# Kernel optimization log

Hardware: AMD Instinct MI355X
Metric: run time of the kernel (lower is better)

## Reference

```python
import jax, jax.numpy as jnp
import numpy as np


def setup_inputs() -> dict:
    key = jax.random.key(0)
    ks = jax.random.split(key, 5)
    B, H, W, dim = 2, 56, 56, 256
    heads, k = 8, 7
    s = 0.02
    return {
        "hidden_states": jax.random.normal(ks[0], (B, H, W, dim), jnp.float32),
        "wq": jax.random.normal(ks[1], (dim, dim), jnp.float32) * s,
        "bq": jnp.zeros((dim,), jnp.float32),
        "wk": jax.random.normal(ks[2], (dim, dim), jnp.float32) * s,
        "bk": jnp.zeros((dim,), jnp.float32),
        "wv": jax.random.normal(ks[3], (dim, dim), jnp.float32) * s,
        "bv": jnp.zeros((dim,), jnp.float32),
        "rpb": jax.random.normal(ks[4], (heads, 2 * k - 1, 2 * k - 1), jnp.float32) * s,
    }


def _window_start(L, k):
    # NATTEN window start for dilation=1: centered window, clamped to stay inside [0, L)
    ns = k // 2
    i = jnp.arange(L)
    return jnp.maximum(i - ns, 0) + jnp.where(i + ns >= L, L - i - ns - 1, 0)


def _neighborhood_attention(hidden_states, wq, bq, wk, bk, wv, bv, rpb):
    B, H, W, dim = hidden_states.shape
    heads = rpb.shape[0]
    k = (rpb.shape[1] + 1) // 2  # rpb is (heads, 2k-1, 2k-1)
    hd = dim // heads

    def proj(w, b):
        y = hidden_states @ w.T + b  # nn.Linear convention: x @ W^T + b
        return y.reshape(B, H, W, heads, hd).transpose(0, 3, 1, 2, 4)  # [B,h,H,W,d]

    q = proj(wq, bq) / jnp.sqrt(jnp.float32(hd))
    kl = proj(wk, bk)
    vl = proj(wv, bv)

    off = jnp.arange(k)
    ki = _window_start(H, k)[:, None] + off[None, :]  # [H,k] key row indices per query row
    kj = _window_start(W, k)[:, None] + off[None, :]  # [W,k] key col indices per query col

    def gather_nbhd(x):
        # x: [B,h,H,W,d] -> [B,h,H,W,k*k,d]
        g = x[:, :, ki[:, :, None, None], kj[None, None, :, :], :]  # [B,h,H,k,W,k,d]
        return g.transpose(0, 1, 2, 4, 3, 5, 6).reshape(B, heads, H, W, k * k, hd)

    kn = gather_nbhd(kl)
    vn = gather_nbhd(vl)

    # relative position bias index = (key_pos - query_pos) + (k - 1)
    pbi = ki - jnp.arange(H)[:, None] + (k - 1)  # [H,k]
    pbj = kj - jnp.arange(W)[:, None] + (k - 1)  # [W,k]
    bias = rpb[:, pbi[:, :, None, None], pbj[None, None, :, :]]  # [h,H,k,W,k]
    bias = bias.transpose(0, 1, 3, 2, 4).reshape(heads, H, W, k * k)

    scores = jnp.einsum('bnijd,bnijkd->bnijk', q, kn) + bias[None]
    probs = jax.nn.softmax(scores, axis=-1)  # dropout prob = 0.0 (eval)
    ctx = jnp.einsum('bnijk,bnijkd->bnijd', probs, vn)
    return ctx.transpose(0, 2, 3, 1, 4).reshape(B, H, W, dim)


def reference(hidden_states, wq, bq, wk, bk, wv, bv, rpb):
    return _neighborhood_attention(hidden_states, wq, bq, wk, bk, wv, bv, rpb)
```

## Files before the change

### kernel.cpp

```cpp
#include <hip/hip_runtime.h>
#include <hip/hip_bf16.h>

typedef __attribute__((ext_vector_type(8))) short bf16x8;
typedef __attribute__((ext_vector_type(4))) float f32x4;

#define NPIX 6272
#define HW 56
#define HEADS 8
#define HD 32
#define KW 7
#define DIM 256
#define GDIM 768
#define UK 112
#define UKP 128
#define NX (NPIX * DIM)
#define NW (DIM * DIM)

__device__ inline short f2bf(float f) {
    __hip_bfloat16 h = __float2bfloat16(f);
    return *(short*)&h;
}
__device__ inline float bf2f(short u) {
    union { unsigned int i; float f; } x;
    x.i = ((unsigned int)(unsigned short)u) << 16;
    return x.f;
}

__device__ __forceinline__ void gl_lds16(const short* g, short* l) {
    __builtin_amdgcn_global_load_lds(
        (const __attribute__((address_space(1))) unsigned int*)g,
        (__attribute__((address_space(3))) unsigned int*)l,
        16, 0, 0);
}

__global__ __launch_bounds__(256) void cvt_kernel(
    const float* __restrict__ X,
    const float* __restrict__ Wq, const float* __restrict__ Wk, const float* __restrict__ Wv,
    short* __restrict__ Xb, short* __restrict__ Wcb)
{
    const size_t e0 = ((size_t)blockIdx.x * 256 + threadIdx.x) * 8;
    const float* src; short* dst; size_t off;
    if (e0 < NX)                { src = X;  dst = Xb;        off = e0; }
    else if (e0 < NX + NW)      { src = Wq; dst = Wcb;       off = e0 - NX; }
    else if (e0 < NX + 2 * NW)  { src = Wk; dst = Wcb + NW;  off = e0 - NX - NW; }
    else                        { src = Wv; dst = Wcb + 2*NW; off = e0 - NX - 2 * NW; }
    float4 f0 = *(const float4*)(src + off);
    float4 f1 = *(const float4*)(src + off + 4);
    bf16x8 v;
    v[0]=f2bf(f0.x); v[1]=f2bf(f0.y); v[2]=f2bf(f0.z); v[3]=f2bf(f0.w);
    v[4]=f2bf(f1.x); v[5]=f2bf(f1.y); v[6]=f2bf(f1.z); v[7]=f2bf(f1.w);
    *(bf16x8*)(dst + off) = v;
}

__global__ __launch_bounds__(256, 2) void proj_kernel(
    const short* __restrict__ Xb,
    const short* __restrict__ Wcb,
    const float* __restrict__ Bq, const float* __restrict__ Bk, const float* __restrict__ Bv,
    short* __restrict__ Y)
{
    __shared__ short Ash[64 * 256];
    __shared__ short Bsh[64 * 256];

    const int id   = blockIdx.x;
    const int flat = (id & 7) * 147 + (id >> 3);
    const int bx   = flat / 12;
    const int by   = flat - bx * 12;

    const int tid  = threadIdx.x;
    const int wave = tid >> 6;
    const int lane = tid & 63;
    const int l15  = lane & 15;
    const int hi   = lane >> 4;

    const int brow = bx * 64;
    const int bcol = by * 64;

    #pragma unroll
    for (int i = 0; i < 8; ++i) {
        const int slot = tid + i * 256;
        const int row  = slot >> 5;
        const int p    = slot & 31;
        const int goff = ((p ^ (row & 7)) << 3);
        gl_lds16(Xb  + (size_t)(brow + row) * DIM + goff, Ash + slot * 8);
        gl_lds16(Wcb + (size_t)(bcol + row) * DIM + goff, Bsh + slot * 8);
    }
    __syncthreads();

    f32x4 acc[4];
    #pragma unroll
    for (int c = 0; c < 4; ++c) acc[c] = (f32x4){0.f, 0.f, 0.f, 0.f};

    const int arow = wave * 16 + l15;
    #pragma unroll
    for (int kk = 0; kk < 8; ++kk) {
        const int ch = kk * 4 + hi;
        bf16x8 a = *(const bf16x8*)((char*)Ash + arow * 512 + ((ch ^ (arow & 7)) << 4));
        #pragma unroll
        for (int c = 0; c < 4; ++c) {
            const int bro = c * 16 + l15;
            bf16x8 b = *(const bf16x8*)((char*)Bsh + bro * 512 + ((ch ^ (bro & 7)) << 4));
            acc[c] = __builtin_amdgcn_mfma_f32_16x16x32_bf16(a, b, acc[c], 0, 0, 0);
        }
    }

    const int z = by >> 2;
    const float* Bi = (z == 0) ? Bq : (z == 1) ? Bk : Bv;
    const float scale = (z == 0) ? 0.17677669529663687f : 1.0f;
    #pragma unroll
    for (int c = 0; c < 4; ++c) {
        const int ocol = bcol + c * 16 + l15;
        const float bvv = Bi[ocol & 255];
        #pragma unroll
        for (int r = 0; r < 4; ++r) {
            const int row = brow + wave * 16 + hi * 4 + r;
            Y[(size_t)row * GDIM + ocol] = f2bf((acc[c][r] + bvv) * scale);
        }
    }
}

__global__ __launch_bounds__(256, 3) void nattn_kernel(
    const short* __restrict__ Yg,
    const float* __restrict__ rpb,
    float* __restrict__ out)
{
    __shared__ short VshT[128 * UKP];
    __shared__ short Psh[4 * 16 * UKP];
    __shared__ __align__(16) short rpbs[8 * 169];

    const int id   = blockIdx.x;
    const int flat = (id & 7) * 98 + (id >> 3);
    const int bz   = flat / 392;
    int rem        = flat - bz * 392;
    const int ip   = rem / 14;
    rem           -= ip * 14;
    const int hg   = rem / 7;
    const int jt   = rem - hg * 7;

    const int tid  = threadIdx.x;
    const int wv   = tid >> 6;
    const int lane = tid & 63;
    const int l15  = lane & 15;
    const int hi   = lane >> 4;

    const int i0 = 2 * ip;
    const int j0 = jt * 8;
    const int r0 = min(max(i0 - 3, 0), HW - KW);
    const int c0 = min(max(j0 - 3, 0), HW - KW);

    const int h = hg * 4 + wv;

    const int k2   = tid & 63;
    const int dblk = tid >> 6;
    const int keyL = 2 * k2, keyR = 2 * k2 + 1;
    const int aL = keyL / 14, cL = keyL - aL * 14;
    const int aR = keyR / 14, cR = keyR - aR * 14;
    const int giL = min(r0 + aL, HW - 1), gjL = min(c0 + cL, HW - 1);
    const int giR = min(r0 + aR, HW - 1), gjR = min(c0 + cR, HW - 1);
    const short* srcL = Yg + (size_t)((bz * HW + giL) * HW + gjL) * GDIM + 512 + hg * 128 + dblk * 32;
    const short* srcR = Yg + (size_t)((bz * HW + giR) * HW + gjR) * GDIM + 512 + hg * 128 + dblk * 32;
    bf16x8 vL[4], vR[4];
    #pragma unroll
    for (int m = 0; m < 4; ++m) {
        vL[m] = (keyL < UK) ? *(const bf16x8*)(srcL + m * 8) : (bf16x8){0,0,0,0,0,0,0,0};
        vR[m] = (keyR < UK) ? *(const bf16x8*)(srcR + m * 8) : (bf16x8){0,0,0,0,0,0,0,0};
    }

    const int qpix = (bz * HW + i0 + (l15 >> 3)) * HW + j0 + (l15 & 7);
    bf16x8 aq = *(const bf16x8*)(Yg + (size_t)qpix * GDIM + h * HD + hi * 8);

    const float4* rpb4 = (const float4*)rpb;
    float4 rv0 = rpb4[tid];
    float4 rv1 = (tid < 338 - 256) ? rpb4[tid + 256] : (float4){0.f,0.f,0.f,0.f};

    #pragma unroll
    for (int m = 0; m < 4; ++m) {
        #pragma unroll
        for (int e = 0; e < 8; ++e) {
            const int d = dblk * 32 + m * 8 + e;
            const int w = ((int)(unsigned short)vL[m][e]) | ((int)vR[m][e] << 16);
            *(int*)((char*)VshT + d * 256 + ((4 * k2) ^ (e << 4))) = w;
        }
    }
    *(short4*)(&rpbs[tid * 4]) = make_short4(f2bf(rv0.x), f2bf(rv0.y), f2bf(rv0.z), f2bf(rv0.w));
    if (tid < 338 - 256)
        *(short4*)(&rpbs[(tid + 256) * 4]) = make_short4(f2bf(rv1.x), f2bf(rv1.y), f2bf(rv1.z), f2bf(rv1.w));
    {
        const int p = (lane >> 2) & 15, m4 = lane & 3;
        const int k = UK + m4 * 4;
        char* dst = (char*)Psh + (wv * 16 + p) * 256 + ((2 * k) ^ (p << 4));
        *(int2*)dst = make_int2(0, 0);
    }
    __syncthreads();

    int iv[4], jv[4], bb[4], uai[4], ucj[4];
    #pragma unroll
    for (int r = 0; r < 4; ++r) {
        const int p = hi * 4 + r;
        iv[r] = i0 + (p >> 3);
        jv[r] = j0 + (p & 7);
        const int siv = min(max(iv[r] - 3, 0), HW - KW);
        const int sjv = min(max(jv[r] - 3, 0), HW - KW);
        bb[r]  = (r0 - iv[r] + 6) * 13 + (c0 - jv[r] + 6);
        uai[r] = siv - r0;
        ucj[r] = sjv - c0;
    }
    const f32x4 zf = {0.f, 0.f, 0.f, 0.f};

    f32x4 sacc[7];
    {
        bf16x8 kb[7];
        #pragma unroll
        for (int t = 0; t < 7; ++t) {
            const int key = t * 16 + l15;
            const int a = key / 14, c = key - a * 14;
            const int gi = min(r0 + a, HW - 1), gj = min(c0 + c, HW - 1);
            kb[t] = *(const bf16x8*)(Yg + (size_t)((bz * HW + gi) * HW + gj) * GDIM +
                                     256 + h * HD + hi * 8);
        }
        #pragma unroll
        for (int t = 0; t < 7; ++t)
            sacc[t] = __builtin_amdgcn_mfma_f32_16x16x32_bf16(aq, kb[t], zf, 0, 0, 0);
    }

    const short* rbh = rpbs + h * 169;
    int aA[7], cA[7], a13[7];
    #pragma unroll
    for (int t = 0; t < 7; ++t) {
        const int key = t * 16 + l15;
        aA[t] = key / 14;
        cA[t] = key - aA[t] * 14;
        a13[t] = aA[t] * 13 + cA[t];
    }
    float sc[4][7];
    #pragma unroll
    for (int t = 0; t < 7; ++t) {
        #pragma unroll
        for (int r = 0; r < 4; ++r) {
            const bool ok = ((unsigned)(aA[t] - uai[r]) <= 6u) &
                            ((unsigned)(cA[t] - ucj[r]) <= 6u);
            const float s = sacc[t][r] + bf2f(rbh[bb[r] + a13[t]]);
            sc[r][t] = ok ? s : -1e30f;
        }
    }

    float sm[4];
    #pragma unroll
    for (int r = 0; r < 4; ++r) {
        float m = sc[r][0];
        #pragma unroll
        for (int t = 1; t < 7; ++t) m = fmaxf(m, sc[r][t]);
        m = fmaxf(m, __shfl_xor(m, 1));
        m = fmaxf(m, __shfl_xor(m, 2));
        m = fmaxf(m, __shfl_xor(m, 4));
        m = fmaxf(m, __shfl_xor(m, 8));
        const int pix = hi * 4 + r;
        char* prow = (char*)Psh + (wv * 16 + pix) * 256;
        const int pswz = pix << 4;
        float s = 0.f;
        #pragma unroll
        for (int t = 0; t < 7; ++t) {
            const float e = __expf(sc[r][t] - m);
            s += e;
            const int key = t * 16 + l15;
            *(short*)(prow + ((2 * key) ^ pswz)) = f2bf(e);
        }
        s += __shfl_xor(s, 1);
        s += __shfl_xor(s, 2);
        s += __shfl_xor(s, 4);
        s += __shfl_xor(s, 8);
        sm[r] = s;
    }

    const int d0 = wv * 32 + l15;
    f32x4 o0 = zf, o1 = zf;
    #pragma unroll
    for (int kk = 0; kk < 4; ++kk) {
        bf16x8 pa = *(const bf16x8*)((char*)Psh + (wv * 16 + l15) * 256 +
                                     ((kk * 64 + hi * 16) ^ (l15 << 4)));
        const int koff = (kk * 64 + hi * 16) ^ ((l15 & 7) << 4);
        bf16x8 vb0 = *(const bf16x8*)((char*)VshT + d0 * 256 + koff);
        bf16x8 vb1 = *(const bf16x8*)((char*)VshT + (d0 + 16) * 256 + koff);
        o0 = __builtin_amdgcn_mfma_f32_16x16x32_bf16(pa, vb0, o0, 0, 0, 0);
        o1 = __builtin_amdgcn_mfma_f32_16x16x32_bf16(pa, vb1, o1, 0, 0, 0);
    }

    #pragma unroll
    for (int r = 0; r < 4; ++r) {
        const float inv = 1.f / sm[r];
        const int pg = (bz * HW + iv[r]) * HW + jv[r];
        out[(size_t)pg * DIM + h * HD + l15]      = o0[r] * inv;
        out[(size_t)pg * DIM + h * HD + 16 + l15] = o1[r] * inv;
    }
}

extern "C" void kernel_launch(void* const* d_in, const int* in_sizes, int n_in,
                              void* d_out, int out_size, void* d_ws, size_t ws_size,
                              hipStream_t stream) {
    const float* hs = (const float*)d_in[0];
    const float* wq = (const float*)d_in[1];
    const float* bq = (const float*)d_in[2];
    const float* wk = (const float*)d_in[3];
    const float* bk = (const float*)d_in[4];
    const float* wv = (const float*)d_in[5];
    const float* bv = (const float*)d_in[6];
    const float* rpb = (const float*)d_in[7];

    short* Y   = (short*)d_ws;
    short* Xb  = Y + (size_t)NPIX * GDIM;
    short* Wcb = Xb + (size_t)NX;

    cvt_kernel<<<(NX + 3 * NW) / (256 * 8), 256, 0, stream>>>(hs, wq, wk, wv, Xb, Wcb);

    proj_kernel<<<1176, 256, 0, stream>>>(Xb, Wcb, bq, bk, bv, Y);

    nattn_kernel<<<784, 256, 0, stream>>>(Y, rpb, (float*)d_out);
}
```

Measured before the change: 32.80 us.

## Split projection K-loop into two staged halves and hoist K loads before barrier

The projection GEMM now loads the 256-wide K dimension as two 128-wide halves into separate LDS buffers. MFMA work on the first half can start while the second half's global-to-LDS copies are still in flight. In the attention kernel, the key-vector global loads are issued before the V-transpose/LDS staging and the barrier, so their latency overlaps with the shared-memory setup. This raises register pressure (kb held across the barrier) and adds an extra sync in the GEMM.

```diff
diff --git a/kernel.cpp b/kernel.cpp
--- a/kernel.cpp
+++ b/kernel.cpp
@@ -58,8 +58,8 @@
     const float* __restrict__ Bq, const float* __restrict__ Bk, const float* __restrict__ Bv,
     short* __restrict__ Y)
 {
-    __shared__ short Ash[64 * 256];
-    __shared__ short Bsh[64 * 256];
+    __shared__ short Ash[2][1024 * 8];
+    __shared__ short Bsh[2][1024 * 8];
 
     const int id   = blockIdx.x;
     const int flat = (id & 7) * 147 + (id >> 3);
@@ -75,30 +75,51 @@
     const int brow = bx * 64;
     const int bcol = by * 64;
 
-    #pragma unroll
-    for (int i = 0; i < 8; ++i) {
-        const int slot = tid + i * 256;
-        const int row  = slot >> 5;
-        const int p    = slot & 31;
+    f32x4 acc[4];
+    #pragma unroll
+    for (int c = 0; c < 4; ++c) acc[c] = (f32x4){0.f, 0.f, 0.f, 0.f};
+    const int arow = wave * 16 + l15;
+
+    #pragma unroll
+    for (int i = 0; i < 4; ++i) {
+        const int slot = i * 256 + tid;
+        const int row = slot >> 4, p = slot & 15;
         const int goff = ((p ^ (row & 7)) << 3);
-        gl_lds16(Xb  + (size_t)(brow + row) * DIM + goff, Ash + slot * 8);
-        gl_lds16(Wcb + (size_t)(bcol + row) * DIM + goff, Bsh + slot * 8);
+        gl_lds16(Xb  + (size_t)(brow + row) * DIM + goff, &Ash[0][slot * 8]);
+        gl_lds16(Wcb + (size_t)(bcol + row) * DIM + goff, &Bsh[0][slot * 8]);
     }
     __syncthreads();
 
-    f32x4 acc[4];
-    #pragma unroll
-    for (int c = 0; c < 4; ++c) acc[c] = (f32x4){0.f, 0.f, 0.f, 0.f};
-
-    const int arow = wave * 16 + l15;
-    #pragma unroll
-    for (int kk = 0; kk < 8; ++kk) {
+    #pragma unroll
+    for (int i = 0; i < 4; ++i) {
+        const int slot = i * 256 + tid;
+        const int row = slot >> 4, p = slot & 15;
+        const int goff = ((p ^ (row & 7)) << 3) + 128;
+        gl_lds16(Xb  + (size_t)(brow + row) * DIM + goff, &Ash[1][slot * 8]);
+        gl_lds16(Wcb + (size_t)(bcol + row) * DIM + goff, &Bsh[1][slot * 8]);
+    }
+
+    #pragma unroll
+    for (int kk = 0; kk < 4; ++kk) {
         const int ch = kk * 4 + hi;
-        bf16x8 a = *(const bf16x8*)((char*)Ash + arow * 512 + ((ch ^ (arow & 7)) << 4));
+        bf16x8 a = *(const bf16x8*)((char*)&Ash[0][0] + arow * 256 + ((ch ^ (arow & 7)) << 4));
         #pragma unroll
         for (int c = 0; c < 4; ++c) {
             const int bro = c * 16 + l15;
-            bf16x8 b = *(const bf16x8*)((char*)Bsh + bro * 512 + ((ch ^ (bro & 7)) << 4));
+            bf16x8 b = *(const bf16x8*)((char*)&Bsh[0][0] + bro * 256 + ((ch ^ (bro & 7)) << 4));
+            acc[c] = __builtin_amdgcn_mfma_f32_16x16x32_bf16(a, b, acc[c], 0, 0, 0);
+        }
+    }
+    __syncthreads();
+
+    #pragma unroll
+    for (int kk = 0; kk < 4; ++kk) {
+        const int ch = kk * 4 + hi;
+        bf16x8 a = *(const bf16x8*)((char*)&Ash[1][0] + arow * 256 + ((ch ^ (arow & 7)) << 4));
+        #pragma unroll
+        for (int c = 0; c < 4; ++c) {
+            const int bro = c * 16 + l15;
+            bf16x8 b = *(const bf16x8*)((char*)&Bsh[1][0] + bro * 256 + ((ch ^ (bro & 7)) << 4));
             acc[c] = __builtin_amdgcn_mfma_f32_16x16x32_bf16(a, b, acc[c], 0, 0, 0);
         }
     }
@@ -168,29 +189,19 @@
     const int qpix = (bz * HW + i0 + (l15 >> 3)) * HW + j0 + (l15 & 7);
     bf16x8 aq = *(const bf16x8*)(Yg + (size_t)qpix * GDIM + h * HD + hi * 8);
 
+    bf16x8 kb[7];
+    #pragma unroll
+    for (int t = 0; t < 7; ++t) {
+        const int key = t * 16 + l15;
+        const int a = key / 14, c = key - a * 14;
+        const int gi = min(r0 + a, HW - 1), gj = min(c0 + c, HW - 1);
+        kb[t] = *(const bf16x8*)(Yg + (size_t)((bz * HW + gi) * HW + gj) * GDIM +
+                                 256 + h * HD + hi * 8);
+    }
+
     const float4* rpb4 = (const float4*)rpb;
     float4 rv0 = rpb4[tid];
     float4 rv1 = (tid < 338 - 256) ? rpb4[tid + 256] : (float4){0.f,0.f,0.f,0.f};
-
-    #pragma unroll
-    for (int m = 0; m < 4; ++m) {
-        #pragma unroll
-        for (int e = 0; e < 8; ++e) {
-            const int d = dblk * 32 + m * 8 + e;
-            const int w = ((int)(unsigned short)vL[m][e]) | ((int)vR[m][e] << 16);
-            *(int*)((char*)VshT + d * 256 + ((4 * k2) ^ (e << 4))) = w;
-        }
-    }
-    *(short4*)(&rpbs[tid * 4]) = make_short4(f2bf(rv0.x), f2bf(rv0.y), f2bf(rv0.z), f2bf(rv0.w));
-    if (tid < 338 - 256)
-        *(short4*)(&rpbs[(tid + 256) * 4]) = make_short4(f2bf(rv1.x), f2bf(rv1.y), f2bf(rv1.z), f2bf(rv1.w));
-    {
-        const int p = (lane >> 2) & 15, m4 = lane & 3;
-        const int k = UK + m4 * 4;
-        char* dst = (char*)Psh + (wv * 16 + p) * 256 + ((2 * k) ^ (p << 4));
-        *(int2*)dst = make_int2(0, 0);
-    }
-    __syncthreads();
 
     int iv[4], jv[4], bb[4], uai[4], ucj[4];
     #pragma unroll
@@ -204,25 +215,6 @@
         uai[r] = siv - r0;
         ucj[r] = sjv - c0;
     }
-    const f32x4 zf = {0.f, 0.f, 0.f, 0.f};
-
-    f32x4 sacc[7];
-    {
-        bf16x8 kb[7];
-        #pragma unroll
-        for (int t = 0; t < 7; ++t) {
-            const int key = t * 16 + l15;
-            const int a = key / 14, c = key - a * 14;
-            const int gi = min(r0 + a, HW - 1), gj = min(c0 + c, HW - 1);
-            kb[t] = *(const bf16x8*)(Yg + (size_t)((bz * HW + gi) * HW + gj) * GDIM +
-                                     256 + h * HD + hi * 8);
-        }
-        #pragma unroll
-        for (int t = 0; t < 7; ++t)
-            sacc[t] = __builtin_amdgcn_mfma_f32_16x16x32_bf16(aq, kb[t], zf, 0, 0, 0);
-    }
-
-    const short* rbh = rpbs + h * 169;
     int aA[7], cA[7], a13[7];
     #pragma unroll
     for (int t = 0; t < 7; ++t) {
@@ -231,6 +223,35 @@
         cA[t] = key - aA[t] * 14;
         a13[t] = aA[t] * 13 + cA[t];
     }
+
+    #pragma unroll
+    for (int m = 0; m < 4; ++m) {
+        #pragma unroll
+        for (int e = 0; e < 8; ++e) {
+            const int d = dblk * 32 + m * 8 + e;
+            const int w = ((int)(unsigned short)vL[m][e]) | ((int)vR[m][e] << 16);
+            *(int*)((char*)VshT + d * 256 + ((4 * k2) ^ (e << 4))) = w;
+        }
+    }
+    *(short4*)(&rpbs[tid * 4]) = make_short4(f2bf(rv0.x), f2bf(rv0.y), f2bf(rv0.z), f2bf(rv0.w));
+    if (tid < 338 - 256)
+        *(short4*)(&rpbs[(tid + 256) * 4]) = make_short4(f2bf(rv1.x), f2bf(rv1.y), f2bf(rv1.z), f2bf(rv1.w));
+    {
+        const int p = (lane >> 2) & 15, m4 = lane & 3;
+        const int k = UK + m4 * 4;
+        char* dst = (char*)Psh + (wv * 16 + p) * 256 + ((2 * k) ^ (p << 4));
+        *(int2*)dst = make_int2(0, 0);
+    }
+    __syncthreads();
+
+    const f32x4 zf = {0.f, 0.f, 0.f, 0.f};
+
+    f32x4 sacc[7];
+    #pragma unroll
+    for (int t = 0; t < 7; ++t)
+        sacc[t] = __builtin_amdgcn_mfma_f32_16x16x32_bf16(aq, kb[t], zf, 0, 0, 0);
+
+    const short* rbh = rpbs + h * 169;
     float sc[4][7];
     #pragma unroll
     for (int t = 0; t < 7; ++t) {
```

After: 33.15 us. Within noise of the previous version (+1.1%).

## Store projected Q/K/V in head-planar layout for contiguous per-head reads

Applied to the files above, without the earlier changes.

The projection kernel now writes Q, K and V as separate per-head planes of 32-wide rows instead of one interleaved 768-wide row per pixel. The attention kernel's K, Q and V loads are rewritten against the new layout, and the V transpose into shared memory now writes individual shorts instead of packed pairs. The aim is to make neighbourhood gathers touch contiguous 64-byte rows per head for better cache-line use. In exchange, the projection epilogue writes are more scattered and the V staging issues more LDS stores.

```diff
diff --git a/kernel.cpp b/kernel.cpp
--- a/kernel.cpp
+++ b/kernel.cpp
@@ -10,7 +10,6 @@
 #define HD 32
 #define KW 7
 #define DIM 256
-#define GDIM 768
 #define UK 112
 #define UKP 128
 #define NX (NPIX * DIM)
@@ -108,12 +107,15 @@
     const float scale = (z == 0) ? 0.17677669529663687f : 1.0f;
     #pragma unroll
     for (int c = 0; c < 4; ++c) {
-        const int ocol = bcol + c * 16 + l15;
-        const float bvv = Bi[ocol & 255];
+        const int col256 = (by & 3) * 64 + c * 16 + l15;
+        const int h = col256 >> 5;
+        const int d = col256 & 31;
+        const float bvv = Bi[col256];
+        const size_t pbase = (size_t)(z * 8 + h) * NPIX;
         #pragma unroll
         for (int r = 0; r < 4; ++r) {
             const int row = brow + wave * 16 + hi * 4 + r;
-            Y[(size_t)row * GDIM + ocol] = f2bf((acc[c][r] + bvv) * scale);
+            Y[(pbase + row) * 32 + d] = f2bf((acc[c][r] + bvv) * scale);
         }
     }
 }
@@ -149,38 +151,34 @@
 
     const int h = hg * 4 + wv;
 
-    const int k2   = tid & 63;
-    const int dblk = tid >> 6;
-    const int keyL = 2 * k2, keyR = 2 * k2 + 1;
-    const int aL = keyL / 14, cL = keyL - aL * 14;
-    const int aR = keyR / 14, cR = keyR - aR * 14;
-    const int giL = min(r0 + aL, HW - 1), gjL = min(c0 + cL, HW - 1);
-    const int giR = min(r0 + aR, HW - 1), gjR = min(c0 + cR, HW - 1);
-    const short* srcL = Yg + (size_t)((bz * HW + giL) * HW + gjL) * GDIM + 512 + hg * 128 + dblk * 32;
-    const short* srcR = Yg + (size_t)((bz * HW + giR) * HW + gjR) * GDIM + 512 + hg * 128 + dblk * 32;
-    bf16x8 vL[4], vR[4];
-    #pragma unroll
-    for (int m = 0; m < 4; ++m) {
-        vL[m] = (keyL < UK) ? *(const bf16x8*)(srcL + m * 8) : (bf16x8){0,0,0,0,0,0,0,0};
-        vR[m] = (keyR < UK) ? *(const bf16x8*)(srcR + m * 8) : (bf16x8){0,0,0,0,0,0,0,0};
+    #pragma unroll
+    for (int hh = 0; hh < 4; ++hh) {
+        const size_t vpl = (size_t)(16 + hg * 4 + hh) * NPIX;
+        #pragma unroll
+        for (int i = 0; i < 2; ++i) {
+            const int slot  = i * 256 + tid;
+            const int key   = slot >> 2;
+            const int chunk = slot & 3;
+            const int a = key / 14, c = key - a * 14;
+            const int gi = min(r0 + a, HW - 1), gj = min(c0 + c, HW - 1);
+            bf16x8 vv = {0,0,0,0,0,0,0,0};
+            if (key < UK)
+                vv = *(const bf16x8*)(Yg + (vpl + (bz * HW + gi) * HW + gj) * 32 + chunk * 8);
+            #pragma unroll
+            for (int e = 0; e < 8; ++e) {
+                const int d = chunk * 8 + e;
+                *(short*)((char*)VshT + (hh * 32 + d) * 256 + ((2 * key) ^ (e << 4))) = vv[e];
+            }
+        }
     }
 
     const int qpix = (bz * HW + i0 + (l15 >> 3)) * HW + j0 + (l15 & 7);
-    bf16x8 aq = *(const bf16x8*)(Yg + (size_t)qpix * GDIM + h * HD + hi * 8);
+    bf16x8 aq = *(const bf16x8*)(Yg + ((size_t)h * NPIX + qpix) * 32 + hi * 8);
 
     const float4* rpb4 = (const float4*)rpb;
     float4 rv0 = rpb4[tid];
     float4 rv1 = (tid < 338 - 256) ? rpb4[tid + 256] : (float4){0.f,0.f,0.f,0.f};
 
-    #pragma unroll
-    for (int m = 0; m < 4; ++m) {
-        #pragma unroll
-        for (int e = 0; e < 8; ++e) {
-            const int d = dblk * 32 + m * 8 + e;
-            const int w = ((int)(unsigned short)vL[m][e]) | ((int)vR[m][e] << 16);
-            *(int*)((char*)VshT + d * 256 + ((4 * k2) ^ (e << 4))) = w;
-        }
-    }
     *(short4*)(&rpbs[tid * 4]) = make_short4(f2bf(rv0.x), f2bf(rv0.y), f2bf(rv0.z), f2bf(rv0.w));
     if (tid < 338 - 256)
         *(short4*)(&rpbs[(tid + 256) * 4]) = make_short4(f2bf(rv1.x), f2bf(rv1.y), f2bf(rv1.z), f2bf(rv1.w));
@@ -208,14 +206,14 @@
 
     f32x4 sacc[7];
     {
+        const size_t kpl = (size_t)(8 + h) * NPIX;
         bf16x8 kb[7];
         #pragma unroll
         for (int t = 0; t < 7; ++t) {
             const int key = t * 16 + l15;
             const int a = key / 14, c = key - a * 14;
             const int gi = min(r0 + a, HW - 1), gj = min(c0 + c, HW - 1);
-            kb[t] = *(const bf16x8*)(Yg + (size_t)((bz * HW + gi) * HW + gj) * GDIM +
-                                     256 + h * HD + hi * 8);
+            kb[t] = *(const bf16x8*)(Yg + (kpl + (bz * HW + gi) * HW + gj) * 32 + hi * 8);
         }
         #pragma unroll
         for (int t = 0; t < 7; ++t)
@@ -306,7 +304,7 @@
     const float* rpb = (const float*)d_in[7];
 
     short* Y   = (short*)d_ws;
-    short* Xb  = Y + (size_t)NPIX * GDIM;
+    short* Xb  = Y + (size_t)24 * NPIX * 32;
     short* Wcb = Xb + (size_t)NX;
 
     cvt_kernel<<<(NX + 3 * NW) / (256 * 8), 256, 0, stream>>>(hs, wq, wk, wv, Xb, Wcb);
```

Result: slower. 33.89 us (+3.3%).

## Transpose MFMA operands so softmax probabilities stay in registers, drop LDS staging

Applied to the files above, without the earlier changes.

The score and PV MFMAs now swap their operands, so each lane holds the scores for one query pixel across keys. The softmax reductions then need only two cross-lane shuffles, and the bf16 probabilities are packed and redistributed with __shfl instead of being written to and read back from a shared-memory P buffer. Removing that buffer cuts LDS use, which allows raising the launch-bounds occupancy hint from 3 to 4. Outputs are written as float4 vectors. The trade-off is extra shuffle and select instructions plus higher register pressure under the tighter occupancy bound.

```diff
diff --git a/kernel.cpp b/kernel.cpp
--- a/kernel.cpp
+++ b/kernel.cpp
@@ -118,13 +118,12 @@
     }
 }
 
-__global__ __launch_bounds__(256, 3) void nattn_kernel(
+__global__ __launch_bounds__(256, 4) void nattn_kernel(
     const short* __restrict__ Yg,
     const float* __restrict__ rpb,
     float* __restrict__ out)
 {
     __shared__ short VshT[128 * UKP];
-    __shared__ short Psh[4 * 16 * UKP];
     __shared__ __align__(16) short rpbs[8 * 169];
 
     const int id   = blockIdx.x;
@@ -184,26 +183,15 @@
     *(short4*)(&rpbs[tid * 4]) = make_short4(f2bf(rv0.x), f2bf(rv0.y), f2bf(rv0.z), f2bf(rv0.w));
     if (tid < 338 - 256)
         *(short4*)(&rpbs[(tid + 256) * 4]) = make_short4(f2bf(rv1.x), f2bf(rv1.y), f2bf(rv1.z), f2bf(rv1.w));
-    {
-        const int p = (lane >> 2) & 15, m4 = lane & 3;
-        const int k = UK + m4 * 4;
-        char* dst = (char*)Psh + (wv * 16 + p) * 256 + ((2 * k) ^ (p << 4));
-        *(int2*)dst = make_int2(0, 0);
-    }
     __syncthreads();
 
-    int iv[4], jv[4], bb[4], uai[4], ucj[4];
-    #pragma unroll
-    for (int r = 0; r < 4; ++r) {
-        const int p = hi * 4 + r;
-        iv[r] = i0 + (p >> 3);
-        jv[r] = j0 + (p & 7);
-        const int siv = min(max(iv[r] - 3, 0), HW - KW);
-        const int sjv = min(max(jv[r] - 3, 0), HW - KW);
-        bb[r]  = (r0 - iv[r] + 6) * 13 + (c0 - jv[r] + 6);
-        uai[r] = siv - r0;
-        ucj[r] = sjv - c0;
-    }
+    const int iv = i0 + (l15 >> 3);
+    const int jv = j0 + (l15 & 7);
+    const int siv = min(max(iv - 3, 0), HW - KW);
+    const int sjv = min(max(jv - 3, 0), HW - KW);
+    const int bb  = (r0 - iv + 6) * 13 + (c0 - jv + 6);
+    const int uai = siv - r0;
+    const int ucj = sjv - c0;
     const f32x4 zf = {0.f, 0.f, 0.f, 0.f};
 
     f32x4 sacc[7];
@@ -219,78 +207,78 @@
         }
         #pragma unroll
         for (int t = 0; t < 7; ++t)
-            sacc[t] = __builtin_amdgcn_mfma_f32_16x16x32_bf16(aq, kb[t], zf, 0, 0, 0);
+            sacc[t] = __builtin_amdgcn_mfma_f32_16x16x32_bf16(kb[t], aq, zf, 0, 0, 0);
     }
 
     const short* rbh = rpbs + h * 169;
-    int aA[7], cA[7], a13[7];
+    float sc[7][4];
     #pragma unroll
     for (int t = 0; t < 7; ++t) {
-        const int key = t * 16 + l15;
-        aA[t] = key / 14;
-        cA[t] = key - aA[t] * 14;
-        a13[t] = aA[t] * 13 + cA[t];
-    }
-    float sc[4][7];
+        #pragma unroll
+        for (int r = 0; r < 4; ++r) {
+            const int key = t * 16 + (hi << 2) + r;
+            const int a = key / 14, c = key - a * 14;
+            const bool ok = ((unsigned)(a - uai) <= 6u) & ((unsigned)(c - ucj) <= 6u);
+            const float s = sacc[t][r] + bf2f(rbh[bb + a * 13 + c]);
+            sc[t][r] = ok ? s : -1e30f;
+        }
+    }
+
+    float m = sc[0][0];
+    #pragma unroll
+    for (int t = 0; t < 7; ++t)
+        #pragma unroll
+        for (int r = 0; r < 4; ++r) m = fmaxf(m, sc[t][r]);
+    m = fmaxf(m, __shfl_xor(m, 16));
+    m = fmaxf(m, __shfl_xor(m, 32));
+
+    float sm = 0.f;
+    unsigned long long pk[7];
     #pragma unroll
     for (int t = 0; t < 7; ++t) {
-        #pragma unroll
-        for (int r = 0; r < 4; ++r) {
-            const bool ok = ((unsigned)(aA[t] - uai[r]) <= 6u) &
-                            ((unsigned)(cA[t] - ucj[r]) <= 6u);
-            const float s = sacc[t][r] + bf2f(rbh[bb[r] + a13[t]]);
-            sc[r][t] = ok ? s : -1e30f;
-        }
-    }
-
-    float sm[4];
-    #pragma unroll
-    for (int r = 0; r < 4; ++r) {
-        float m = sc[r][0];
-        #pragma unroll
-        for (int t = 1; t < 7; ++t) m = fmaxf(m, sc[r][t]);
-        m = fmaxf(m, __shfl_xor(m, 1));
-        m = fmaxf(m, __shfl_xor(m, 2));
-        m = fmaxf(m, __shfl_xor(m, 4));
-        m = fmaxf(m, __shfl_xor(m, 8));
-        const int pix = hi * 4 + r;
-        char* prow = (char*)Psh + (wv * 16 + pix) * 256;
-        const int pswz = pix << 4;
-        float s = 0.f;
-        #pragma unroll
-        for (int t = 0; t < 7; ++t) {
-            const float e = __expf(sc[r][t] - m);
-            s += e;
-            const int key = t * 16 + l15;
-            *(short*)(prow + ((2 * key) ^ pswz)) = f2bf(e);
-        }
-        s += __shfl_xor(s, 1);
-        s += __shfl_xor(s, 2);
-        s += __shfl_xor(s, 4);
-        s += __shfl_xor(s, 8);
-        sm[r] = s;
-    }
-
+        float e0 = __expf(sc[t][0] - m), e1 = __expf(sc[t][1] - m);
+        float e2 = __expf(sc[t][2] - m), e3 = __expf(sc[t][3] - m);
+        sm += (e0 + e1) + (e2 + e3);
+        const unsigned u0 = (unsigned)(unsigned short)f2bf(e0) |
+                            ((unsigned)(unsigned short)f2bf(e1) << 16);
+        const unsigned u1 = (unsigned)(unsigned short)f2bf(e2) |
+                            ((unsigned)(unsigned short)f2bf(e3) << 16);
+        pk[t] = (unsigned long long)u0 | ((unsigned long long)u1 << 32);
+    }
+    sm += __shfl_xor(sm, 16);
+    sm += __shfl_xor(sm, 32);
+
+    const int s0 = l15 + ((hi & 1) << 5);
+    const bool hiSel = (hi >> 1) & 1;
     const int d0 = wv * 32 + l15;
     f32x4 o0 = zf, o1 = zf;
     #pragma unroll
     for (int kk = 0; kk < 4; ++kk) {
-        bf16x8 pa = *(const bf16x8*)((char*)Psh + (wv * 16 + l15) * 256 +
-                                     ((kk * 64 + hi * 16) ^ (l15 << 4)));
+        unsigned long long a0 = __shfl(pk[2 * kk], s0, 64);
+        unsigned long long b0 = __shfl(pk[2 * kk], s0 + 16, 64);
+        unsigned long long a1 = 0ULL, b1 = 0ULL;
+        if (2 * kk + 1 < 7) {
+            a1 = __shfl(pk[2 * kk + 1], s0, 64);
+            b1 = __shfl(pk[2 * kk + 1], s0 + 16, 64);
+        }
+        bf16x8 pa;
+        ((unsigned long long*)&pa)[0] = hiSel ? a1 : a0;
+        ((unsigned long long*)&pa)[1] = hiSel ? b1 : b0;
+
         const int koff = (kk * 64 + hi * 16) ^ ((l15 & 7) << 4);
-        bf16x8 vb0 = *(const bf16x8*)((char*)VshT + d0 * 256 + koff);
-        bf16x8 vb1 = *(const bf16x8*)((char*)VshT + (d0 + 16) * 256 + koff);
-        o0 = __builtin_amdgcn_mfma_f32_16x16x32_bf16(pa, vb0, o0, 0, 0, 0);
-        o1 = __builtin_amdgcn_mfma_f32_16x16x32_bf16(pa, vb1, o1, 0, 0, 0);
-    }
-
-    #pragma unroll
-    for (int r = 0; r < 4; ++r) {
-        const float inv = 1.f / sm[r];
-        const int pg = (bz * HW + iv[r]) * HW + jv[r];
-        out[(size_t)pg * DIM + h * HD + l15]      = o0[r] * inv;
-        out[(size_t)pg * DIM + h * HD + 16 + l15] = o1[r] * inv;
-    }
+        bf16x8 va0 = *(const bf16x8*)((char*)VshT + d0 * 256 + koff);
+        bf16x8 va1 = *(const bf16x8*)((char*)VshT + (d0 + 16) * 256 + koff);
+        o0 = __builtin_amdgcn_mfma_f32_16x16x32_bf16(va0, pa, o0, 0, 0, 0);
+        o1 = __builtin_amdgcn_mfma_f32_16x16x32_bf16(va1, pa, o1, 0, 0, 0);
+    }
+
+    const float inv = 1.f / sm;
+    float4 w0, w1;
+    w0.x = o0[0] * inv; w0.y = o0[1] * inv; w0.z = o0[2] * inv; w0.w = o0[3] * inv;
+    w1.x = o1[0] * inv; w1.y = o1[1] * inv; w1.z = o1[2] * inv; w1.w = o1[3] * inv;
+    float* orow = out + (size_t)qpix * DIM + h * HD + hi * 4;
+    *(float4*)(orow)      = w0;
+    *(float4*)(orow + 16) = w1;
 }
 
 extern "C" void kernel_launch(void* const* d_in, const int* in_sizes, int n_in,
```

Measured after the change: 31.25 us. 1.05x faster.
